# Kernel tuning notes

Measured on AMD Instinct MI355X. Metric: run time of the kernel, lower is better.

## Reference

```python
import jax, jax.numpy as jnp
import numpy as np

B, N, N_IN, N_HID, EIN = 8, 256, 64, 128, 16


def setup_inputs() -> dict:
    key = jax.random.key(0)
    ks = jax.random.split(key, 12)
    s_in = 1.0 / np.sqrt(N_IN)
    s_e = 1.0 / np.sqrt(EIN)
    s_h = 1.0 / np.sqrt(N_HID)
    return {
        "x": jax.random.normal(ks[0], (B, N, N_IN), jnp.float32),
        "e": jax.random.normal(ks[1], (B, N, N, EIN), jnp.float32),
        "Wf": jax.random.uniform(ks[2], (N_IN, N_HID), jnp.float32, -s_in, s_in),
        "bf": jax.random.uniform(ks[3], (N_HID,), jnp.float32, -s_in, s_in),
        "Wt": jax.random.uniform(ks[4], (N_IN, N_HID), jnp.float32, -s_in, s_in),
        "bt": jax.random.uniform(ks[5], (N_HID,), jnp.float32, -s_in, s_in),
        "We": jax.random.uniform(ks[6], (EIN, N_HID), jnp.float32, -s_e, s_e),
        "be": jax.random.uniform(ks[7], (N_HID,), jnp.float32, -s_e, s_e),
        "W1": jax.random.uniform(ks[8], (N_HID, N_HID), jnp.float32, -s_h, s_h),
        "b1": jax.random.uniform(ks[9], (N_HID,), jnp.float32, -s_h, s_h),
        "W2": jax.random.uniform(ks[10], (N_HID, N_IN), jnp.float32, -s_h, s_h),
        "b2": jax.random.uniform(ks[11], (N_IN,), jnp.float32, -s_h, s_h),
    }


def reference(x, e, Wf, bf, Wt, bt, We, be, W1, b1, W2, b2):
    # x: [B,N,F], e: [B,N,N,E]
    n = x.shape[1]
    ne_f = x @ Wf + bf                      # [B,N,H] (node_emb_1)
    ne_t = x @ Wt + bt                      # [B,N,H] (node_emb_2)
    ee = e @ We + be                        # [B,N,N,H]
    # pair[b,i,j] = node_emb_1[b,j] + node_emb_2[b,i] + edge_emb[b,i,j]
    pair = ne_f[:, None, :, :] + ne_t[:, :, None, :] + ee
    # zero the diagonal (both node_emb and edge_emb diagonals were zeroed)
    mask = (1.0 - jnp.eye(n, dtype=x.dtype))[None, :, :, None]
    node_emb = jax.nn.relu(pair * mask).mean(axis=2)  # [B,N,H]
    h = jax.nn.relu(node_emb @ W1 + b1)
    return h @ W2 + b2 + x
```

## Files before the change

kernel.cpp:

```cpp
#include <hip/hip_runtime.h>
#include <hip/hip_bf16.h>


#define BB 8
#define NN 256
#define FF 64
#define HH 128
#define EE 16

typedef __attribute__((ext_vector_type(8))) short bf16x8;
typedef __attribute__((ext_vector_type(16))) float f32x16;

__device__ __forceinline__ short f2bf(float f) {
    union { float f; unsigned u; } v; v.f = f;
    unsigned r = v.u + 0x7FFFu + ((v.u >> 16) & 1u);
    return (short)(r >> 16);
}
__device__ __forceinline__ float bf2f(short s) {
    union { unsigned u; float f; } v; v.u = ((unsigned)(unsigned short)s) << 16;
    return v.f;
}

__global__ __launch_bounds__(128) void k_node_emb(
    const float* __restrict__ x,
    const float* __restrict__ Wf, const float* __restrict__ bf,
    const float* __restrict__ Wt, const float* __restrict__ bt,
    const float* __restrict__ be,
    float* __restrict__ nef, float* __restrict__ net)
{
    __shared__ float smx[4 * FF];
    const int tid = threadIdx.x;
    const int row0 = blockIdx.x * 4;

    smx[tid]       = x[(size_t)row0 * FF + tid];
    smx[tid + 128] = x[(size_t)row0 * FF + tid + 128];
    __syncthreads();

    const int h = tid;
    const float bsum = bf[h] + bt[h] + be[h];
    float af0 = 0.f, af1 = 0.f, af2 = 0.f, af3 = 0.f;
    float at0 = bsum, at1 = bsum, at2 = bsum, at3 = bsum;

    #pragma unroll 8
    for (int k = 0; k < FF; ++k) {
        const float wf = Wf[k * HH + h];
        const float wt = Wt[k * HH + h];
        const float x0 = smx[k], x1 = smx[FF + k], x2 = smx[2 * FF + k], x3 = smx[3 * FF + k];
        af0 = fmaf(x0, wf, af0); af1 = fmaf(x1, wf, af1);
        af2 = fmaf(x2, wf, af2); af3 = fmaf(x3, wf, af3);
        at0 = fmaf(x0, wt, at0); at1 = fmaf(x1, wt, at1);
        at2 = fmaf(x2, wt, at2); at3 = fmaf(x3, wt, at3);
    }
    nef[(size_t)(row0 + 0) * HH + h] = af0;
    nef[(size_t)(row0 + 1) * HH + h] = af1;
    nef[(size_t)(row0 + 2) * HH + h] = af2;
    nef[(size_t)(row0 + 3) * HH + h] = af3;
    net[(size_t)(row0 + 0) * HH + h] = at0;
    net[(size_t)(row0 + 1) * HH + h] = at1;
    net[(size_t)(row0 + 2) * HH + h] = at2;
    net[(size_t)(row0 + 3) * HH + h] = at3;
}

__global__ __launch_bounds__(256) void k_pair_mfma(
    const float* __restrict__ x, const float* __restrict__ e,
    const float* __restrict__ We,
    const float* __restrict__ nef, const float* __restrict__ net,
    const float* __restrict__ W1, const float* __restrict__ b1,
    const float* __restrict__ W2, const float* __restrict__ b2,
    float* __restrict__ out)
{
    const int row  = blockIdx.x;
    const int b    = row >> 8;
    const int i    = row & (NN - 1);
    const int tid  = threadIdx.x;
    const int wave = tid >> 6;
    const int lane = tid & 63;
    const int c    = lane & 31;
    const int half = lane >> 5;

    __shared__ float smred[4][HH];
    __shared__ float sm_ne[HH];
    __shared__ float sm_h1[HH];

    bf16x8 bfrag[4];
    #pragma unroll
    for (int ht = 0; ht < 4; ++ht) {
        bf16x8 t;
        #pragma unroll
        for (int el = 0; el < 8; ++el) {
            const int k = 8 * half + el;
            t[el] = f2bf(We[k * HH + ht * 32 + c]);
        }
        bfrag[ht] = t;
    }

    float netv[4];
    #pragma unroll
    for (int ht = 0; ht < 4; ++ht) netv[ht] = net[(size_t)row * HH + ht * 32 + c];

    const float* __restrict__ eRow = e + (size_t)row * (NN * EE);
    const float* __restrict__ nefb = nef + (size_t)b * (NN * HH);

    float acc[4] = {0.f, 0.f, 0.f, 0.f};

    #pragma unroll
    for (int q = 0; q < 2; ++q) {
        const int jt = wave * 2 + q;
        const int j  = jt * 32 + c;
        const float4* ap = (const float4*)(eRow + (size_t)j * EE + 8 * half);
        const float4 p0 = ap[0];
        const float4 p1 = ap[1];
        bf16x8 afrag;
        afrag[0] = f2bf(p0.x); afrag[1] = f2bf(p0.y);
        afrag[2] = f2bf(p0.z); afrag[3] = f2bf(p0.w);
        afrag[4] = f2bf(p1.x); afrag[5] = f2bf(p1.y);
        afrag[6] = f2bf(p1.z); afrag[7] = f2bf(p1.w);

        #pragma unroll
        for (int ht = 0; ht < 4; ++ht) {
            f32x16 d = {0.f,0.f,0.f,0.f,0.f,0.f,0.f,0.f,0.f,0.f,0.f,0.f,0.f,0.f,0.f,0.f};
            d = __builtin_amdgcn_mfma_f32_32x32x16_bf16(afrag, bfrag[ht], d, 0, 0, 0);
            #pragma unroll
            for (int r = 0; r < 16; ++r) {
                const int rowj = (r & 3) + 8 * (r >> 2) + 4 * half;
                const float v = d[r] + netv[ht]
                              + nefb[(size_t)(jt * 32 + rowj) * HH + ht * 32 + c];
                acc[ht] += fmaxf(v, 0.f);
            }
        }
    }

    #pragma unroll
    for (int ht = 0; ht < 4; ++ht) acc[ht] += __shfl_xor(acc[ht], 32);
    if (lane < 32) {
        #pragma unroll
        for (int ht = 0; ht < 4; ++ht) smred[wave][ht * 32 + c] = acc[ht];
    }
    __syncthreads();

    if (tid < HH) {
        const int h = tid;
        float s = smred[0][h] + smred[1][h] + smred[2][h] + smred[3][h];
        float dd = nefb[(size_t)i * HH + h] + net[(size_t)row * HH + h];
        const float* ed = eRow + (size_t)i * EE;
        #pragma unroll
        for (int k = 0; k < EE; ++k) {
            dd = fmaf(bf2f(f2bf(ed[k])), bf2f(f2bf(We[k * HH + h])), dd);
        }
        s -= fmaxf(dd, 0.f);
        sm_ne[h] = s * (1.0f / (float)NN);
    }
    __syncthreads();

    if (tid < HH) {
        const int h = tid;
        float a1 = b1[h];
        #pragma unroll 4
        for (int k = 0; k < HH; ++k) a1 = fmaf(sm_ne[k], W1[k * HH + h], a1);
        sm_h1[h] = fmaxf(a1, 0.f);
    }
    __syncthreads();

    if (tid < FF) {
        const int h = tid;
        float a2 = b2[h] + x[(size_t)row * FF + h];
        #pragma unroll 4
        for (int k = 0; k < HH; ++k) a2 = fmaf(sm_h1[k], W2[k * FF + h], a2);
        out[(size_t)row * FF + h] = a2;
    }
}

extern "C" void kernel_launch(void* const* d_in, const int* in_sizes, int n_in,
                              void* d_out, int out_size, void* d_ws, size_t ws_size,
                              hipStream_t stream) {
    (void)in_sizes; (void)n_in; (void)out_size; (void)ws_size;
    const float* x  = (const float*)d_in[0];
    const float* e  = (const float*)d_in[1];
    const float* Wf = (const float*)d_in[2];
    const float* bf = (const float*)d_in[3];
    const float* Wt = (const float*)d_in[4];
    const float* bt = (const float*)d_in[5];
    const float* We = (const float*)d_in[6];
    const float* be = (const float*)d_in[7];
    const float* W1 = (const float*)d_in[8];
    const float* b1 = (const float*)d_in[9];
    const float* W2 = (const float*)d_in[10];
    const float* b2 = (const float*)d_in[11];
    float* out = (float*)d_out;

    float* nef = (float*)d_ws;
    float* net = nef + (size_t)BB * NN * HH;

    k_node_emb<<<(BB * NN) / 4, 128, 0, stream>>>(x, Wf, bf, Wt, bt, be, nef, net);
    k_pair_mfma<<<BB * NN, 256, 0, stream>>>(x, e, We, nef, net, W1, b1, W2, b2, out);
}
```

Measured before the change: 129.2 us.

## Fold node_emb_1 projection into pair MFMA via concatenated x and e operands

Instead of precomputing nef in fp32 and gathering it per (j,h) in the inner loop, the pair kernel now computes x_j@Wf with four extra bf16 MFMAs per tile, concatenating x with e along the K dimension. B fragments for We and Wf are pre-packed into bf16 lane layout by a new pack kernel, and the net bias is used as the MFMA accumulator initial value. This removes the heavy strided nef global loads (128 floats per j per row) at the cost of 5x the MFMA work, x in bf16 precision for the Wf term, and one extra launch.

```diff
diff --git a/kernel.cpp b/kernel.cpp
--- a/kernel.cpp
+++ b/kernel.cpp
@@ -7,6 +7,7 @@
 #define FF 64
 #define HH 128
 #define EE 16
+#define NCH 5
 
 typedef __attribute__((ext_vector_type(8))) short bf16x8;
 typedef __attribute__((ext_vector_type(16))) float f32x16;
@@ -21,12 +22,28 @@
     return v.f;
 }
 
-__global__ __launch_bounds__(128) void k_node_emb(
+__global__ __launch_bounds__(256) void k_pack(
+    const float* __restrict__ We, const float* __restrict__ Wf,
+    short* __restrict__ Bpack)
+{
+    const int total = NCH * 4 * 64 * 8;
+    for (int t = blockIdx.x * 256 + threadIdx.x; t < total; t += gridDim.x * 256) {
+        const int el   = t & 7;
+        const int lane = (t >> 3) & 63;
+        const int ht   = (t >> 9) & 3;
+        const int ch   = t >> 11;
+        const int kl   = 8 * (lane >> 5) + el;
+        const int h    = ht * 32 + (lane & 31);
+        const float v  = (ch == 0) ? We[kl * HH + h] : Wf[(16 * (ch - 1) + kl) * HH + h];
+        Bpack[t] = f2bf(v);
+    }
+}
+
+__global__ __launch_bounds__(128) void k_prep(
     const float* __restrict__ x,
-    const float* __restrict__ Wf, const float* __restrict__ bf,
-    const float* __restrict__ Wt, const float* __restrict__ bt,
-    const float* __restrict__ be,
-    float* __restrict__ nef, float* __restrict__ net)
+    const float* __restrict__ Wt,
+    const float* __restrict__ bf, const float* __restrict__ bt, const float* __restrict__ be,
+    float* __restrict__ net, short* __restrict__ xbf)
 {
     __shared__ float smx[4 * FF];
     const int tid = threadIdx.x;
@@ -38,33 +55,31 @@
 
     const int h = tid;
     const float bsum = bf[h] + bt[h] + be[h];
-    float af0 = 0.f, af1 = 0.f, af2 = 0.f, af3 = 0.f;
-    float at0 = bsum, at1 = bsum, at2 = bsum, at3 = bsum;
+    float a0 = bsum, a1 = bsum, a2 = bsum, a3 = bsum;
 
     #pragma unroll 8
     for (int k = 0; k < FF; ++k) {
-        const float wf = Wf[k * HH + h];
         const float wt = Wt[k * HH + h];
-        const float x0 = smx[k], x1 = smx[FF + k], x2 = smx[2 * FF + k], x3 = smx[3 * FF + k];
-        af0 = fmaf(x0, wf, af0); af1 = fmaf(x1, wf, af1);
-        af2 = fmaf(x2, wf, af2); af3 = fmaf(x3, wf, af3);
-        at0 = fmaf(x0, wt, at0); at1 = fmaf(x1, wt, at1);
-        at2 = fmaf(x2, wt, at2); at3 = fmaf(x3, wt, at3);
-    }
-    nef[(size_t)(row0 + 0) * HH + h] = af0;
-    nef[(size_t)(row0 + 1) * HH + h] = af1;
-    nef[(size_t)(row0 + 2) * HH + h] = af2;
-    nef[(size_t)(row0 + 3) * HH + h] = af3;
-    net[(size_t)(row0 + 0) * HH + h] = at0;
-    net[(size_t)(row0 + 1) * HH + h] = at1;
-    net[(size_t)(row0 + 2) * HH + h] = at2;
-    net[(size_t)(row0 + 3) * HH + h] = at3;
+        a0 = fmaf(smx[k], wt, a0);
+        a1 = fmaf(smx[FF + k], wt, a1);
+        a2 = fmaf(smx[2 * FF + k], wt, a2);
+        a3 = fmaf(smx[3 * FF + k], wt, a3);
+    }
+    net[(size_t)(row0 + 0) * HH + h] = a0;
+    net[(size_t)(row0 + 1) * HH + h] = a1;
+    net[(size_t)(row0 + 2) * HH + h] = a2;
+    net[(size_t)(row0 + 3) * HH + h] = a3;
+
+    const int r = tid >> 6, f = tid & 63;
+    xbf[(size_t)(row0 + r) * FF + f]     = f2bf(smx[r * FF + f]);
+    xbf[(size_t)(row0 + r + 2) * FF + f] = f2bf(smx[(r + 2) * FF + f]);
 }
 
 __global__ __launch_bounds__(256) void k_pair_mfma(
     const float* __restrict__ x, const float* __restrict__ e,
-    const float* __restrict__ We,
-    const float* __restrict__ nef, const float* __restrict__ net,
+    const float* __restrict__ We, const float* __restrict__ Wf,
+    const float* __restrict__ net, const short* __restrict__ xbf,
+    const short* __restrict__ Bpack,
     const float* __restrict__ W1, const float* __restrict__ b1,
     const float* __restrict__ W2, const float* __restrict__ b2,
     float* __restrict__ out)
@@ -82,24 +97,20 @@
     __shared__ float sm_ne[HH];
     __shared__ float sm_h1[HH];
 
-    bf16x8 bfrag[4];
-    #pragma unroll
-    for (int ht = 0; ht < 4; ++ht) {
-        bf16x8 t;
-        #pragma unroll
-        for (int el = 0; el < 8; ++el) {
-            const int k = 8 * half + el;
-            t[el] = f2bf(We[k * HH + ht * 32 + c]);
-        }
-        bfrag[ht] = t;
-    }
+    const bf16x8* __restrict__ bp = (const bf16x8*)Bpack;
+    bf16x8 bfrag[NCH][4];
+    #pragma unroll
+    for (int ch = 0; ch < NCH; ++ch)
+        #pragma unroll
+        for (int ht = 0; ht < 4; ++ht)
+            bfrag[ch][ht] = bp[(ch * 4 + ht) * 64 + lane];
 
     float netv[4];
     #pragma unroll
     for (int ht = 0; ht < 4; ++ht) netv[ht] = net[(size_t)row * HH + ht * 32 + c];
 
     const float* __restrict__ eRow = e + (size_t)row * (NN * EE);
-    const float* __restrict__ nefb = nef + (size_t)b * (NN * HH);
+    const short* __restrict__ xb   = xbf + (size_t)b * (NN * FF);
 
     float acc[4] = {0.f, 0.f, 0.f, 0.f};
 
@@ -107,26 +118,31 @@
     for (int q = 0; q < 2; ++q) {
         const int jt = wave * 2 + q;
         const int j  = jt * 32 + c;
+
         const float4* ap = (const float4*)(eRow + (size_t)j * EE + 8 * half);
         const float4 p0 = ap[0];
         const float4 p1 = ap[1];
-        bf16x8 afrag;
-        afrag[0] = f2bf(p0.x); afrag[1] = f2bf(p0.y);
-        afrag[2] = f2bf(p0.z); afrag[3] = f2bf(p0.w);
-        afrag[4] = f2bf(p1.x); afrag[5] = f2bf(p1.y);
-        afrag[6] = f2bf(p1.z); afrag[7] = f2bf(p1.w);
+        bf16x8 ae;
+        ae[0] = f2bf(p0.x); ae[1] = f2bf(p0.y); ae[2] = f2bf(p0.z); ae[3] = f2bf(p0.w);
+        ae[4] = f2bf(p1.x); ae[5] = f2bf(p1.y); ae[6] = f2bf(p1.z); ae[7] = f2bf(p1.w);
+
+        const bf16x8* xp = (const bf16x8*)(xb + (size_t)j * FF + 8 * half);
+        bf16x8 ax0 = xp[0];
+        bf16x8 ax1 = xp[2];
+        bf16x8 ax2 = xp[4];
+        bf16x8 ax3 = xp[6];
 
         #pragma unroll
         for (int ht = 0; ht < 4; ++ht) {
-            f32x16 d = {0.f,0.f,0.f,0.f,0.f,0.f,0.f,0.f,0.f,0.f,0.f,0.f,0.f,0.f,0.f,0.f};
-            d = __builtin_amdgcn_mfma_f32_32x32x16_bf16(afrag, bfrag[ht], d, 0, 0, 0);
+            const float nv = netv[ht];
+            f32x16 d = {nv,nv,nv,nv, nv,nv,nv,nv, nv,nv,nv,nv, nv,nv,nv,nv};
+            d = __builtin_amdgcn_mfma_f32_32x32x16_bf16(ae,  bfrag[0][ht], d, 0, 0, 0);
+            d = __builtin_amdgcn_mfma_f32_32x32x16_bf16(ax0, bfrag[1][ht], d, 0, 0, 0);
+            d = __builtin_amdgcn_mfma_f32_32x32x16_bf16(ax1, bfrag[2][ht], d, 0, 0, 0);
+            d = __builtin_amdgcn_mfma_f32_32x32x16_bf16(ax2, bfrag[3][ht], d, 0, 0, 0);
+            d = __builtin_amdgcn_mfma_f32_32x32x16_bf16(ax3, bfrag[4][ht], d, 0, 0, 0);
             #pragma unroll
-            for (int r = 0; r < 16; ++r) {
-                const int rowj = (r & 3) + 8 * (r >> 2) + 4 * half;
-                const float v = d[r] + netv[ht]
-                              + nefb[(size_t)(jt * 32 + rowj) * HH + ht * 32 + c];
-                acc[ht] += fmaxf(v, 0.f);
-            }
+            for (int r = 0; r < 16; ++r) acc[ht] += fmaxf(d[r], 0.f);
         }
     }
 
@@ -141,12 +157,15 @@
     if (tid < HH) {
         const int h = tid;
         float s = smred[0][h] + smred[1][h] + smred[2][h] + smred[3][h];
-        float dd = nefb[(size_t)i * HH + h] + net[(size_t)row * HH + h];
+        float dd = net[(size_t)row * HH + h];
         const float* ed = eRow + (size_t)i * EE;
         #pragma unroll
-        for (int k = 0; k < EE; ++k) {
+        for (int k = 0; k < EE; ++k)
             dd = fmaf(bf2f(f2bf(ed[k])), bf2f(f2bf(We[k * HH + h])), dd);
-        }
+        const short* xd = xb + (size_t)i * FF;
+        #pragma unroll 8
+        for (int f = 0; f < FF; ++f)
+            dd = fmaf(bf2f(xd[f]), bf2f(f2bf(Wf[f * HH + h])), dd);
         s -= fmaxf(dd, 0.f);
         sm_ne[h] = s * (1.0f / (float)NN);
     }
@@ -188,9 +207,12 @@
     const float* b2 = (const float*)d_in[11];
     float* out = (float*)d_out;
 
-    float* nef = (float*)d_ws;
-    float* net = nef + (size_t)BB * NN * HH;
-
-    k_node_emb<<<(BB * NN) / 4, 128, 0, stream>>>(x, Wf, bf, Wt, bt, be, nef, net);
-    k_pair_mfma<<<BB * NN, 256, 0, stream>>>(x, e, We, nef, net, W1, b1, W2, b2, out);
-}
+    float* net   = (float*)d_ws;
+    short* xbf   = (short*)((char*)d_ws + (size_t)BB * NN * HH * 4);
+    short* Bpack = (short*)((char*)d_ws + (size_t)BB * NN * HH * 4 + (size_t)BB * NN * FF * 2);
+
+    k_pack<<<16, 256, 0, stream>>>(We, Wf, Bpack);
+    k_prep<<<(BB * NN) / 4, 128, 0, stream>>>(x, Wt, bf, bt, be, net, xbf);
+    k_pair_mfma<<<BB * NN, 256, 0, stream>>>(x, e, We, Wf, net, xbf, Bpack,
+                                             W1, b1, W2, b2, out);
+}
```

Measured after the change: 162.9 us. 26.1% more time.
